# Performance work log

Measured on AMD Instinct MI355X. Metric: run time of the kernel, lower is better.

Reference implementation:

```python
import jax, jax.numpy as jnp
import numpy as np

B, S, D, H = 2, 2048, 768, 12
DK = D // H  # 64
LN_EPS = 1e-5


def setup_inputs() -> dict:
    key = jax.random.key(0)
    ks = jax.random.split(key, 8)
    std = 0.02
    return {
        "x": jax.random.normal(ks[0], (B, S, D), dtype=jnp.float32),
        "Wq": jax.random.normal(ks[1], (D, D), dtype=jnp.float32) * std,
        "Wp": jax.random.normal(ks[2], (D, D), dtype=jnp.float32) * std,
        "Wk": jax.random.normal(ks[3], (D, D), dtype=jnp.float32) * std,
        "Wv": jax.random.normal(ks[4], (D, D), dtype=jnp.float32) * std,
        "Wo": jax.random.normal(ks[5], (D, D), dtype=jnp.float32) * std,
        "bo": jnp.zeros((D,), dtype=jnp.float32),
        "gamma": jnp.ones((D,), dtype=jnp.float32),
        "beta": jnp.zeros((D,), dtype=jnp.float32),
        "dt": jnp.asarray(0.1, dtype=jnp.float32),
        "gate": jnp.ones((1,), dtype=jnp.float32),
    }


def _heads(t):
    # [B,S,D] -> [B,H,S,DK]
    return t.reshape(B, S, H, DK).transpose(0, 2, 1, 3)


def reference(x, Wq, Wp, Wk, Wv, Wo, bo, gamma, beta, dt, gate):
    scale = DK ** -0.5
    q = _heads(x @ Wq)
    p = _heads(x @ Wp)
    k = _heads(x @ Wk)
    v = _heads(x @ Wv)

    # --- first attention pass (potential energy at q) ---
    e1 = jnp.einsum("bhsd,bhtd->bhst", q, k) * scale
    w1 = jax.nn.softmax(e1, axis=-1)
    pe1 = jnp.einsum("bhst,bhtd->bhsd", w1, v)  # dV/dq approx (v_to_k = Identity since d_v == d_k)

    # --- leapfrog half step + full position step ---
    p_half = p - (dt / 2) * pe1 * gate
    q_new = q + dt * p_half

    # --- second attention pass at updated q ---
    e2 = jnp.einsum("bhsd,bhtd->bhst", q_new, k) * scale
    w2 = jax.nn.softmax(e2, axis=-1)
    pe2 = jnp.einsum("bhst,bhtd->bhsd", w2, v)
    p_new = p_half - (dt / 2) * pe2 * gate

    q_flat = q_new.transpose(0, 2, 1, 3).reshape(B, S, D)
    out = q_flat @ Wo + bo + x  # to_output + residual

    mu = jnp.mean(out, axis=-1, keepdims=True)
    var = jnp.mean(jnp.square(out - mu), axis=-1, keepdims=True)
    return (out - mu) * jax.lax.rsqrt(var + LN_EPS) * gamma + beta
```

## Files before the change

kernel.cpp:

```cpp
#include <hip/hip_runtime.h>
#include <stdint.h>

typedef __bf16 bf16;
typedef __bf16 bf16x8 __attribute__((ext_vector_type(8)));
typedef __bf16 bf16x4 __attribute__((ext_vector_type(4)));
typedef float f32x4 __attribute__((ext_vector_type(4)));

constexpr int nB = 2, nS = 2048, nD = 768, nH = 12, nDK = 64;
constexpr int nM = nB * nS;
constexpr float LN_EPS = 1e-5f;

static __device__ __forceinline__ f32x4 mfma16(bf16x8 a, bf16x8 b, f32x4 c) {
  return __builtin_amdgcn_mfma_f32_16x16x32_bf16(a, b, c, 0, 0, 0);
}

static __device__ __forceinline__ void gll16(const void* g, void* l) {
  __builtin_amdgcn_global_load_lds(
      (const __attribute__((address_space(1))) void*)g,
      (__attribute__((address_space(3))) void*)l, 16, 0, 0);
}

__global__ __launch_bounds__(256) void k_prep_x(const float* __restrict__ x,
                                                bf16* __restrict__ xb) {
  int i = (blockIdx.x * 256 + threadIdx.x) * 4;
  float4 v = *(const float4*)(x + i);
  bf16x4 o;
  o[0] = (bf16)v.x; o[1] = (bf16)v.y; o[2] = (bf16)v.z; o[3] = (bf16)v.w;
  *(bf16x4*)(xb + i) = o;
}

__global__ __launch_bounds__(256) void k_prep_w(
    const float* __restrict__ w0, const float* __restrict__ w1,
    const float* __restrict__ w2, const float* __restrict__ w3,
    const float* __restrict__ w4, bf16* __restrict__ wt) {
  __shared__ float tb[64][65];
  int w = blockIdx.z;
  const float* src = (w == 0) ? w0 : (w == 1) ? w1 : (w == 2) ? w2 : (w == 3) ? w3 : w4;
  int k0 = blockIdx.y * 64, n0 = blockIdx.x * 64;
  int tx = threadIdx.x & 63, ty = threadIdx.x >> 6;
#pragma unroll
  for (int it = 0; it < 16; ++it) {
    int r = it * 4 + ty;
    tb[r][tx] = src[(size_t)(k0 + r) * nD + n0 + tx];
  }
  __syncthreads();
  bf16* dst = wt + (size_t)w * nD * nD;
#pragma unroll
  for (int it = 0; it < 16; ++it) {
    int r = it * 4 + ty;
    dst[(size_t)(n0 + r) * nD + k0 + tx] = (bf16)tb[tx][r];
  }
}

__global__ __launch_bounds__(256) void k_gemm_qpkv(
    const bf16* __restrict__ xb, const bf16* __restrict__ wt,
    bf16* __restrict__ qf, bf16* __restrict__ pf, bf16* __restrict__ kf_,
    bf16* __restrict__ vt) {
  __shared__ alignas(16) char smem[32768];
  char* As = smem;
  char* Bs = smem + 16384;
  int t = threadIdx.x, lane = t & 63, w = t >> 6;
  int fr = lane & 15, fg = lane >> 4;
  int wm = w >> 1, wn = w & 1;
  int widx = blockIdx.z;
  int m0 = blockIdx.y * 128, n0 = blockIdx.x * 128;
  const bf16* wbase = wt + (size_t)widx * nD * nD;
  int srow = t >> 3;
  int scol = (t & 7) * 8;

  f32x4 acc[4][4];
#pragma unroll
  for (int i = 0; i < 4; ++i)
#pragma unroll
    for (int j = 0; j < 4; ++j) acc[i][j] = (f32x4){0.f, 0.f, 0.f, 0.f};

  for (int kt = 0; kt < nD / 64; ++kt) {
    int k0 = kt * 64;
#pragma unroll
    for (int inst = 0; inst < 4; ++inst) {
      int row = inst * 32 + srow;
      int phys = row * 128 + (((t & 7) * 16) ^ ((row & 7) << 4));
      *(bf16x8*)(As + phys) = *(const bf16x8*)(xb + (size_t)(m0 + row) * nD + k0 + scol);
      *(bf16x8*)(Bs + phys) = *(const bf16x8*)(wbase + (size_t)(n0 + row) * nD + k0 + scol);
    }
    __syncthreads();
#pragma unroll
    for (int ks = 0; ks < 2; ++ks) {
      bf16x8 af[4], bfr[4];
#pragma unroll
      for (int i = 0; i < 4; ++i) {
        int row = wm * 64 + i * 16 + fr;
        af[i] = *(const bf16x8*)(As + row * 128 + ((ks * 64 + fg * 16) ^ ((row & 7) << 4)));
      }
#pragma unroll
      for (int j = 0; j < 4; ++j) {
        int row = wn * 64 + j * 16 + fr;
        bfr[j] = *(const bf16x8*)(Bs + row * 128 + ((ks * 64 + fg * 16) ^ ((row & 7) << 4)));
      }
#pragma unroll
      for (int i = 0; i < 4; ++i)
#pragma unroll
        for (int j = 0; j < 4; ++j) acc[i][j] = mfma16(af[i], bfr[j], acc[i][j]);
    }
    __syncthreads();
  }
  if (widx < 3) {
    bf16* outf = (widx == 0) ? qf : (widx == 1) ? pf : kf_;
#pragma unroll
    for (int i = 0; i < 4; ++i)
#pragma unroll
      for (int j = 0; j < 4; ++j) {
        int n = n0 + wn * 64 + j * 16 + fr;
#pragma unroll
        for (int r = 0; r < 4; ++r) {
          int m = m0 + wm * 64 + i * 16 + fg * 4 + r;
          outf[(size_t)m * nD + n] = (bf16)acc[i][j][r];
        }
      }
  } else {
#pragma unroll
    for (int i = 0; i < 4; ++i)
#pragma unroll
      for (int j = 0; j < 4; ++j) {
        int n = n0 + wn * 64 + j * 16 + fr;
        int h = n >> 6, dk = n & 63;
        int mbase = m0 + wm * 64 + i * 16 + fg * 4;
        int b = mbase >> 11, s = mbase & (nS - 1);
        int bh = b * nH + h;
        bf16x4 pk;
#pragma unroll
        for (int r = 0; r < 4; ++r) pk[r] = (bf16)acc[i][j][r];
        *(bf16x4*)(vt + ((size_t)bh * nDK + dk) * nS + s) = pk;
      }
  }
}

__global__ __launch_bounds__(256) void k_attn(
    const bf16* __restrict__ qf, const bf16* __restrict__ pf,
    const bf16* __restrict__ kf_, const bf16* __restrict__ vt,
    const float* __restrict__ dtp, const float* __restrict__ gatep,
    bf16* __restrict__ qn) {
  __shared__ alignas(16) char lds[40960];
  char* kb0_ = lds;
  char* kb1_ = lds + 8192;
  char* vb0_ = lds + 16384;
  char* vb1_ = lds + 24576;
  char* plbase = lds + 32768;

  int t = threadIdx.x, lane = t & 63, w = t >> 6;
  int fr = lane & 15, fg = lane >> 4;
  int blk = blockIdx.x;
  int qt = blk & 31, bh = blk >> 5;
  int b = bh / nH, h = bh % nH;
  int q0 = qt * 64 + w * 16;
  const bf16* Qrow = qf + (size_t)(b * nS) * nD + (size_t)h * nDK;
  const bf16* Prow = pf + (size_t)(b * nS) * nD + (size_t)h * nDK;
  const bf16* Krow = kf_ + (size_t)(b * nS) * nD + (size_t)h * nDK;
  const bf16* Vb = vt + (size_t)bh * nDK * nS;
  char* myp = plbase + w * 2048;

  bf16x8 qa[2];
#pragma unroll
  for (int ks = 0; ks < 2; ++ks)
    qa[ks] = *(const bf16x8*)(Qrow + (size_t)(q0 + fr) * nD + ks * 32 + fg * 8);

  float mr = -1e30f, lr = 0.f;
  f32x4 o[4];
#pragma unroll
  for (int df = 0; df < 4; ++df) o[df] = (f32x4){0.f, 0.f, 0.f, 0.f};

  const float sc = 0.125f;
  int rsub = lane >> 3, cir = lane & 7;

#define STAGE(bK, bV, kt)                                                      \
  {                                                                            \
    _Pragma("unroll") for (int i = 0; i < 2; ++i) {                            \
      int row = w * 16 + i * 8 + rsub;                                         \
      int c = cir ^ (row & 7);                                                 \
      gll16(Krow + (size_t)((kt)*64 + row) * nD + c * 8,                       \
            (bK) + w * 2048 + i * 1024);                                       \
      gll16(Vb + (size_t)row * nS + (kt)*64 + c * 8,                           \
            (bV) + w * 2048 + i * 1024);                                       \
    }                                                                          \
  }

#define COMPUTE(bK, bV)                                                        \
  {                                                                            \
    f32x4 sf[4];                                                               \
    _Pragma("unroll") for (int kfi = 0; kfi < 4; ++kfi) {                      \
      int key = kfi * 16 + fr;                                                 \
      bf16x8 ka = *(const bf16x8*)((bK) + key * 128 + ((fg ^ (key & 7)) << 4));\
      bf16x8 kc =                                                              \
          *(const bf16x8*)((bK) + key * 128 + (((4 + fg) ^ (key & 7)) << 4));  \
      f32x4 sacc = mfma16(ka, qa[0], (f32x4){0.f, 0.f, 0.f, 0.f});             \
      sf[kfi] = mfma16(kc, qa[1], sacc);                                       \
    }                                                                          \
    float mx = -1e30f;                                                         \
    _Pragma("unroll") for (int kfi = 0; kfi < 4; ++kfi)                        \
        _Pragma("unroll") for (int r = 0; r < 4; ++r) mx =                     \
        fmaxf(mx, sf[kfi][r]);                                                 \
    mx = fmaxf(mx, __shfl_xor(mx, 16));                                        \
    mx = fmaxf(mx, __shfl_xor(mx, 32));                                        \
    float mn = fmaxf(mr, mx * sc);                                             \
    float rs = __expf(mr - mn);                                                \
    float e[4][4];                                                             \
    float ts = 0.f;                                                            \
    _Pragma("unroll") for (int kfi = 0; kfi < 4; ++kfi)                        \
        _Pragma("unroll") for (int r = 0; r < 4; ++r) {                        \
      float v = __expf(__builtin_fmaf(sf[kfi][r], sc, -mn));                   \
      e[kfi][r] = v;                                                           \
      ts += v;                                                                 \
    }                                                                          \
    ts += __shfl_xor(ts, 16);                                                  \
    ts += __shfl_xor(ts, 32);                                                  \
    lr = lr * rs + ts;                                                         \
    mr = mn;                                                                   \
    _Pragma("unroll") for (int df = 0; df < 4; ++df) o[df] *= rs;              \
    _Pragma("unroll") for (int kfi = 0; kfi < 4; ++kfi) {                      \
      bf16x4 pk;                                                               \
      _Pragma("unroll") for (int r = 0; r < 4; ++r) pk[r] = (bf16)e[kfi][r];   \
      int blk16 = kfi * 2 + (fg >> 1);                                         \
      int phys = fr * 128 + (((blk16 ^ (fr & 7)) << 4) | ((fg & 1) << 3));     \
      *(bf16x4*)(myp + phys) = pk;                                             \
    }                                                                          \
    _Pragma("unroll") for (int ks = 0; ks < 2; ++ks) {                         \
      bf16x8 pb =                                                              \
          *(const bf16x8*)(myp + fr * 128 + (((ks * 4 + fg) ^ (fr & 7)) << 4));\
      _Pragma("unroll") for (int df = 0; df < 4; ++df) {                       \
        int row = df * 16 + fr;                                                \
        bf16x8 vv = *(const bf16x8*)((bV) + row * 128 +                        \
                                     (((ks * 4 + fg) ^ (row & 7)) << 4));      \
        o[df] = mfma16(vv, pb, o[df]);                                         \
      }                                                                        \
    }                                                                          \
  }

  STAGE(kb0_, vb0_, 0);
  __syncthreads();
#pragma unroll 1
  for (int kt = 0; kt < 32; kt += 2) {
    STAGE(kb1_, vb1_, kt + 1);
    COMPUTE(kb0_, vb0_);
    __syncthreads();
    if (kt + 2 < 32) STAGE(kb0_, vb0_, kt + 2);
    COMPUTE(kb1_, vb1_);
    __syncthreads();
  }
#undef STAGE
#undef COMPUTE

  float dt = dtp[0], gate = gatep[0];
  float c2 = 0.5f * dt * dt * gate;
  float inv = 1.f / lr;
  int qrow = q0 + fr;
#pragma unroll
  for (int df = 0; df < 4; ++df) {
    int dk = df * 16 + fg * 4;
    bf16x4 qv4 = *(const bf16x4*)(Qrow + (size_t)qrow * nD + dk);
    bf16x4 pv4 = *(const bf16x4*)(Prow + (size_t)qrow * nD + dk);
    bf16x4 ov;
#pragma unroll
    for (int r = 0; r < 4; ++r) {
      float pe = o[df][r] * inv;
      ov[r] = (bf16)((float)qv4[r] + dt * (float)pv4[r] - c2 * pe);
    }
    *(bf16x4*)(qn + ((size_t)(b * nS) + qrow) * nD + h * nDK + dk) = ov;
  }
}

__global__ __launch_bounds__(256) void k_gemm_out(
    const bf16* __restrict__ qn, const bf16* __restrict__ wto,
    const float* __restrict__ bo, const float* __restrict__ x,
    float* __restrict__ outp) {
  __shared__ alignas(16) char smem[32768];
  char* As = smem;
  char* Bs = smem + 16384;
  int t = threadIdx.x, lane = t & 63, w = t >> 6;
  int fr = lane & 15, fg = lane >> 4;
  int wm = w >> 1, wn = w & 1;
  int m0 = blockIdx.y * 128, n0 = blockIdx.x * 128;
  int srow = t >> 3;
  int scol = (t & 7) * 8;

  f32x4 acc[4][4];
#pragma unroll
  for (int i = 0; i < 4; ++i)
#pragma unroll
    for (int j = 0; j < 4; ++j) acc[i][j] = (f32x4){0.f, 0.f, 0.f, 0.f};

  for (int kt = 0; kt < nD / 64; ++kt) {
    int k0 = kt * 64;
#pragma unroll
    for (int inst = 0; inst < 4; ++inst) {
      int row = inst * 32 + srow;
      int phys = row * 128 + (((t & 7) * 16) ^ ((row & 7) << 4));
      *(bf16x8*)(As + phys) = *(const bf16x8*)(qn + (size_t)(m0 + row) * nD + k0 + scol);
      *(bf16x8*)(Bs + phys) = *(const bf16x8*)(wto + (size_t)(n0 + row) * nD + k0 + scol);
    }
    __syncthreads();
#pragma unroll
    for (int ks = 0; ks < 2; ++ks) {
      bf16x8 af[4], bfr[4];
#pragma unroll
      for (int i = 0; i < 4; ++i) {
        int row = wm * 64 + i * 16 + fr;
        af[i] = *(const bf16x8*)(As + row * 128 + ((ks * 64 + fg * 16) ^ ((row & 7) << 4)));
      }
#pragma unroll
      for (int j = 0; j < 4; ++j) {
        int row = wn * 64 + j * 16 + fr;
        bfr[j] = *(const bf16x8*)(Bs + row * 128 + ((ks * 64 + fg * 16) ^ ((row & 7) << 4)));
      }
#pragma unroll
      for (int i = 0; i < 4; ++i)
#pragma unroll
        for (int j = 0; j < 4; ++j) acc[i][j] = mfma16(af[i], bfr[j], acc[i][j]);
    }
    __syncthreads();
  }
#pragma unroll
  for (int i = 0; i < 4; ++i)
#pragma unroll
    for (int j = 0; j < 4; ++j) {
      int n = n0 + wn * 64 + j * 16 + fr;
      float bias = bo[n];
#pragma unroll
      for (int r = 0; r < 4; ++r) {
        int m = m0 + wm * 64 + i * 16 + fg * 4 + r;
        outp[(size_t)m * nD + n] = acc[i][j][r] + bias + x[(size_t)m * nD + n];
      }
    }
}

__global__ __launch_bounds__(256) void k_ln(const float* outp,
                                            const float* __restrict__ gamma,
                                            const float* __restrict__ beta,
                                            float* y) {
  int t = threadIdx.x, lane = t & 63, w = t >> 6;
  int row = blockIdx.x * 4 + w;
  const float* rp = outp + (size_t)row * nD;
  float v[12], s1 = 0.f, s2 = 0.f;
#pragma unroll
  for (int i = 0; i < 12; ++i) {
    v[i] = rp[lane + i * 64];
    s1 += v[i];
    s2 += v[i] * v[i];
  }
#pragma unroll
  for (int d = 1; d < 64; d <<= 1) {
    s1 += __shfl_xor(s1, d);
    s2 += __shfl_xor(s2, d);
  }
  float mu = s1 * (1.f / 768.f);
  float var = s2 * (1.f / 768.f) - mu * mu;
  float rstd = rsqrtf(var + LN_EPS);
  float* yp = y + (size_t)row * nD;
#pragma unroll
  for (int i = 0; i < 12; ++i) {
    int n = lane + i * 64;
    yp[n] = (v[i] - mu) * rstd * gamma[n] + beta[n];
  }
}

extern "C" void kernel_launch(void* const* d_in, const int* in_sizes, int n_in,
                              void* d_out, int out_size, void* d_ws, size_t ws_size,
                              hipStream_t stream) {
  const float* x = (const float*)d_in[0];
  const float* Wq = (const float*)d_in[1];
  const float* Wp = (const float*)d_in[2];
  const float* Wk = (const float*)d_in[3];
  const float* Wv = (const float*)d_in[4];
  const float* Wo = (const float*)d_in[5];
  const float* bo = (const float*)d_in[6];
  const float* gamma = (const float*)d_in[7];
  const float* beta = (const float*)d_in[8];
  const float* dt = (const float*)d_in[9];
  const float* gate = (const float*)d_in[10];

  char* ws = (char*)d_ws;
  const size_t szb = (size_t)nM * nD * 2;
  bf16* xb = (bf16*)(ws + 0 * szb);
  bf16* qf = (bf16*)(ws + 1 * szb);
  bf16* pf = (bf16*)(ws + 2 * szb);
  bf16* kf_ = (bf16*)(ws + 3 * szb);
  bf16* vt = (bf16*)(ws + 4 * szb);
  bf16* wt = (bf16*)(ws + 5 * szb);
  bf16* qn = xb;
  float* outp = (float*)d_out;

  k_prep_x<<<dim3(nM * nD / 1024), dim3(256), 0, stream>>>(x, xb);
  k_prep_w<<<dim3(12, 12, 5), dim3(256), 0, stream>>>(Wq, Wp, Wk, Wv, Wo, wt);
  k_gemm_qpkv<<<dim3(6, 32, 4), dim3(256), 0, stream>>>(xb, wt, qf, pf, kf_, vt);
  k_attn<<<dim3(768), dim3(256), 0, stream>>>(qf, pf, kf_, vt, dt, gate, qn);
  k_gemm_out<<<dim3(6, 32), dim3(256), 0, stream>>>(qn, wt + 4 * (size_t)nD * nD, bo, x, outp);
  k_ln<<<dim3(nM / 4), dim3(256), 0, stream>>>(outp, gamma, beta, (float*)d_out);
}
```

Measured before the change: 124.3 us.

## Double-buffer GEMMs with direct global-to-LDS loads and streamline attention softmax

Both projection GEMMs now load tiles straight from global memory into LDS with global_load_lds into a double buffer, so the next K tile is fetched while the current one is computed. In the attention kernel, scores are pre-scaled by log2(e) so exp2 can be used, and the running max is only rescaled when the new max exceeds the old one by a threshold. The row-sum reduction across lanes is deferred to after the loop. s_setprio hints raise wave priority around the MFMA blocks. Using twice the LDS in the GEMMs may lower occupancy, and the lazy rescale lets exponent values grow by up to 2^4 before renormalising.

```diff
diff --git a/kernel.cpp b/kernel.cpp
--- a/kernel.cpp
+++ b/kernel.cpp
@@ -18,6 +18,16 @@
   __builtin_amdgcn_global_load_lds(
       (const __attribute__((address_space(1))) void*)g,
       (__attribute__((address_space(3))) void*)l, 16, 0, 0);
+}
+
+static __device__ __forceinline__ void stage128x64(const bf16* src, int ldk,
+                                                   char* dst, int t, int w) {
+#pragma unroll
+  for (int i = 0; i < 4; ++i) {
+    int row = i * 32 + (t >> 3);
+    int c = (t & 7) ^ (row & 7);
+    gll16(src + (size_t)row * ldk + c * 8, dst + i * 4096 + w * 1024);
+  }
 }
 
 __global__ __launch_bounds__(256) void k_prep_x(const float* __restrict__ x,
@@ -56,17 +66,14 @@
     const bf16* __restrict__ xb, const bf16* __restrict__ wt,
     bf16* __restrict__ qf, bf16* __restrict__ pf, bf16* __restrict__ kf_,
     bf16* __restrict__ vt) {
-  __shared__ alignas(16) char smem[32768];
-  char* As = smem;
-  char* Bs = smem + 16384;
+  __shared__ alignas(16) char smem[65536];
   int t = threadIdx.x, lane = t & 63, w = t >> 6;
   int fr = lane & 15, fg = lane >> 4;
   int wm = w >> 1, wn = w & 1;
   int widx = blockIdx.z;
   int m0 = blockIdx.y * 128, n0 = blockIdx.x * 128;
-  const bf16* wbase = wt + (size_t)widx * nD * nD;
-  int srow = t >> 3;
-  int scol = (t & 7) * 8;
+  const bf16* abase = xb + (size_t)m0 * nD;
+  const bf16* bbase = wt + (size_t)widx * nD * nD + (size_t)n0 * nD;
 
   f32x4 acc[4][4];
 #pragma unroll
@@ -74,33 +81,37 @@
 #pragma unroll
     for (int j = 0; j < 4; ++j) acc[i][j] = (f32x4){0.f, 0.f, 0.f, 0.f};
 
-  for (int kt = 0; kt < nD / 64; ++kt) {
-    int k0 = kt * 64;
-#pragma unroll
-    for (int inst = 0; inst < 4; ++inst) {
-      int row = inst * 32 + srow;
-      int phys = row * 128 + (((t & 7) * 16) ^ ((row & 7) << 4));
-      *(bf16x8*)(As + phys) = *(const bf16x8*)(xb + (size_t)(m0 + row) * nD + k0 + scol);
-      *(bf16x8*)(Bs + phys) = *(const bf16x8*)(wbase + (size_t)(n0 + row) * nD + k0 + scol);
-    }
-    __syncthreads();
+  stage128x64(abase, nD, smem, t, w);
+  stage128x64(bbase, nD, smem + 16384, t, w);
+  __syncthreads();
+#pragma unroll 1
+  for (int kt = 0; kt < 12; ++kt) {
+    if (kt < 11) {
+      char* nb = smem + ((kt + 1) & 1) * 32768;
+      stage128x64(abase + (kt + 1) * 64, nD, nb, t, w);
+      stage128x64(bbase + (kt + 1) * 64, nD, nb + 16384, t, w);
+    }
+    char* Ab = smem + (kt & 1) * 32768;
+    char* Bb = Ab + 16384;
 #pragma unroll
     for (int ks = 0; ks < 2; ++ks) {
       bf16x8 af[4], bfr[4];
 #pragma unroll
       for (int i = 0; i < 4; ++i) {
         int row = wm * 64 + i * 16 + fr;
-        af[i] = *(const bf16x8*)(As + row * 128 + ((ks * 64 + fg * 16) ^ ((row & 7) << 4)));
+        af[i] = *(const bf16x8*)(Ab + row * 128 + (((ks * 4 + fg) ^ (row & 7)) << 4));
       }
 #pragma unroll
       for (int j = 0; j < 4; ++j) {
         int row = wn * 64 + j * 16 + fr;
-        bfr[j] = *(const bf16x8*)(Bs + row * 128 + ((ks * 64 + fg * 16) ^ ((row & 7) << 4)));
-      }
+        bfr[j] = *(const bf16x8*)(Bb + row * 128 + (((ks * 4 + fg) ^ (row & 7)) << 4));
+      }
+      __builtin_amdgcn_s_setprio(1);
 #pragma unroll
       for (int i = 0; i < 4; ++i)
 #pragma unroll
         for (int j = 0; j < 4; ++j) acc[i][j] = mfma16(af[i], bfr[j], acc[i][j]);
+      __builtin_amdgcn_s_setprio(0);
     }
     __syncthreads();
   }
@@ -169,7 +180,7 @@
 #pragma unroll
   for (int df = 0; df < 4; ++df) o[df] = (f32x4){0.f, 0.f, 0.f, 0.f};
 
-  const float sc = 0.125f;
+  const float sc2 = 0.125f * 1.44269504f;
   int rsub = lane >> 3, cir = lane & 7;
 
 #define STAGE(bK, bV, kt)                                                      \
@@ -187,6 +198,7 @@
 #define COMPUTE(bK, bV)                                                        \
   {                                                                            \
     f32x4 sf[4];                                                               \
+    __builtin_amdgcn_s_setprio(1);                                             \
     _Pragma("unroll") for (int kfi = 0; kfi < 4; ++kfi) {                      \
       int key = kfi * 16 + fr;                                                 \
       bf16x8 ka = *(const bf16x8*)((bK) + key * 128 + ((fg ^ (key & 7)) << 4));\
@@ -195,34 +207,38 @@
       f32x4 sacc = mfma16(ka, qa[0], (f32x4){0.f, 0.f, 0.f, 0.f});             \
       sf[kfi] = mfma16(kc, qa[1], sacc);                                       \
     }                                                                          \
-    float mx = -1e30f;                                                         \
-    _Pragma("unroll") for (int kfi = 0; kfi < 4; ++kfi)                        \
-        _Pragma("unroll") for (int r = 0; r < 4; ++r) mx =                     \
-        fmaxf(mx, sf[kfi][r]);                                                 \
-    mx = fmaxf(mx, __shfl_xor(mx, 16));                                        \
-    mx = fmaxf(mx, __shfl_xor(mx, 32));                                        \
-    float mn = fmaxf(mr, mx * sc);                                             \
-    float rs = __expf(mr - mn);                                                \
-    float e[4][4];                                                             \
-    float ts = 0.f;                                                            \
+    __builtin_amdgcn_s_setprio(0);                                             \
+    float a_[4][4];                                                            \
+    float mx2 = -3e38f;                                                        \
     _Pragma("unroll") for (int kfi = 0; kfi < 4; ++kfi)                        \
         _Pragma("unroll") for (int r = 0; r < 4; ++r) {                        \
-      float v = __expf(__builtin_fmaf(sf[kfi][r], sc, -mn));                   \
-      e[kfi][r] = v;                                                           \
-      ts += v;                                                                 \
-    }                                                                          \
-    ts += __shfl_xor(ts, 16);                                                  \
-    ts += __shfl_xor(ts, 32);                                                  \
-    lr = lr * rs + ts;                                                         \
-    mr = mn;                                                                   \
-    _Pragma("unroll") for (int df = 0; df < 4; ++df) o[df] *= rs;              \
+      float v2 = sf[kfi][r] * sc2;                                             \
+      a_[kfi][r] = v2;                                                         \
+      mx2 = fmaxf(mx2, v2);                                                    \
+    }                                                                          \
+    mx2 = fmaxf(mx2, __shfl_xor(mx2, 16));                                     \
+    mx2 = fmaxf(mx2, __shfl_xor(mx2, 32));                                     \
+    if (__any(mx2 > mr + 4.f)) {                                               \
+      float mn = fmaxf(mr, mx2);                                               \
+      float rs = __builtin_exp2f(mr - mn);                                     \
+      lr *= rs;                                                                \
+      _Pragma("unroll") for (int df = 0; df < 4; ++df) o[df] *= rs;            \
+      mr = mn;                                                                 \
+    }                                                                          \
+    float ts = 0.f;                                                            \
     _Pragma("unroll") for (int kfi = 0; kfi < 4; ++kfi) {                      \
       bf16x4 pk;                                                               \
-      _Pragma("unroll") for (int r = 0; r < 4; ++r) pk[r] = (bf16)e[kfi][r];   \
+      _Pragma("unroll") for (int r = 0; r < 4; ++r) {                          \
+        float e = __builtin_exp2f(a_[kfi][r] - mr);                            \
+        ts += e;                                                               \
+        pk[r] = (bf16)e;                                                       \
+      }                                                                        \
       int blk16 = kfi * 2 + (fg >> 1);                                         \
       int phys = fr * 128 + (((blk16 ^ (fr & 7)) << 4) | ((fg & 1) << 3));     \
       *(bf16x4*)(myp + phys) = pk;                                             \
     }                                                                          \
+    lr += ts;                                                                  \
+    __builtin_amdgcn_s_setprio(1);                                             \
     _Pragma("unroll") for (int ks = 0; ks < 2; ++ks) {                         \
       bf16x8 pb =                                                              \
           *(const bf16x8*)(myp + fr * 128 + (((ks * 4 + fg) ^ (fr & 7)) << 4));\
@@ -233,6 +249,7 @@
         o[df] = mfma16(vv, pb, o[df]);                                         \
       }                                                                        \
     }                                                                          \
+    __builtin_amdgcn_s_setprio(0);                                             \
   }
 
   STAGE(kb0_, vb0_, 0);
@@ -249,6 +266,9 @@
 #undef STAGE
 #undef COMPUTE
 
+  lr += __shfl_xor(lr, 16);
+  lr += __shfl_xor(lr, 32);
+
   float dt = dtp[0], gate = gatep[0];
   float c2 = 0.5f * dt * dt * gate;
   float inv = 1.f / lr;
@@ -272,15 +292,13 @@
     const bf16* __restrict__ qn, const bf16* __restrict__ wto,
     const float* __restrict__ bo, const float* __restrict__ x,
     float* __restrict__ outp) {
-  __shared__ alignas(16) char smem[32768];
-  char* As = smem;
-  char* Bs = smem + 16384;
+  __shared__ alignas(16) char smem[65536];
   int t = threadIdx.x, lane = t & 63, w = t >> 6;
   int fr = lane & 15, fg = lane >> 4;
   int wm = w >> 1, wn = w & 1;
   int m0 = blockIdx.y * 128, n0 = blockIdx.x * 128;
-  int srow = t >> 3;
-  int scol = (t & 7) * 8;
+  const bf16* abase = qn + (size_t)m0 * nD;
+  const bf16* bbase = wto + (size_t)n0 * nD;
 
   f32x4 acc[4][4];
 #pragma unroll
@@ -288,33 +306,37 @@
 #pragma unroll
     for (int j = 0; j < 4; ++j) acc[i][j] = (f32x4){0.f, 0.f, 0.f, 0.f};
 
-  for (int kt = 0; kt < nD / 64; ++kt) {
-    int k0 = kt * 64;
-#pragma unroll
-    for (int inst = 0; inst < 4; ++inst) {
-      int row = inst * 32 + srow;
-      int phys = row * 128 + (((t & 7) * 16) ^ ((row & 7) << 4));
-      *(bf16x8*)(As + phys) = *(const bf16x8*)(qn + (size_t)(m0 + row) * nD + k0 + scol);
-      *(bf16x8*)(Bs + phys) = *(const bf16x8*)(wto + (size_t)(n0 + row) * nD + k0 + scol);
-    }
-    __syncthreads();
+  stage128x64(abase, nD, smem, t, w);
+  stage128x64(bbase, nD, smem + 16384, t, w);
+  __syncthreads();
+#pragma unroll 1
+  for (int kt = 0; kt < 12; ++kt) {
+    if (kt < 11) {
+      char* nb = smem + ((kt + 1) & 1) * 32768;
+      stage128x64(abase + (kt + 1) * 64, nD, nb, t, w);
+      stage128x64(bbase + (kt + 1) * 64, nD, nb + 16384, t, w);
+    }
+    char* Ab = smem + (kt & 1) * 32768;
+    char* Bb = Ab + 16384;
 #pragma unroll
     for (int ks = 0; ks < 2; ++ks) {
       bf16x8 af[4], bfr[4];
 #pragma unroll
       for (int i = 0; i < 4; ++i) {
         int row = wm * 64 + i * 16 + fr;
-        af[i] = *(const bf16x8*)(As + row * 128 + ((ks * 64 + fg * 16) ^ ((row & 7) << 4)));
+        af[i] = *(const bf16x8*)(Ab + row * 128 + (((ks * 4 + fg) ^ (row & 7)) << 4));
       }
 #pragma unroll
       for (int j = 0; j < 4; ++j) {
         int row = wn * 64 + j * 16 + fr;
-        bfr[j] = *(const bf16x8*)(Bs + row * 128 + ((ks * 64 + fg * 16) ^ ((row & 7) << 4)));
-      }
+        bfr[j] = *(const bf16x8*)(Bb + row * 128 + (((ks * 4 + fg) ^ (row & 7)) << 4));
+      }
+      __builtin_amdgcn_s_setprio(1);
 #pragma unroll
       for (int i = 0; i < 4; ++i)
 #pragma unroll
         for (int j = 0; j < 4; ++j) acc[i][j] = mfma16(af[i], bfr[j], acc[i][j]);
+      __builtin_amdgcn_s_setprio(0);
     }
     __syncthreads();
   }
```

New measurement: 125.0 us. No clear change (+0.6%).
